# Kernel tuning notes

Measured on AMD Instinct MI355X. Metric: run time of the kernel, lower is better.

## Reference

```python
import jax, jax.numpy as jnp
import numpy as np

N, A, OBS, H, E, ITERS = 2000, 16, 64, 128, 16000, 8


def _init_linear(key, din, dout):
    kw, kb = jax.random.split(key)
    s = 1.0 / np.sqrt(din)
    W = jax.random.uniform(kw, (dout, din), minval=-s, maxval=s, dtype=jnp.float32)
    b = jax.random.uniform(kb, (dout,), minval=-s, maxval=s, dtype=jnp.float32)
    return W, b


def setup_inputs() -> dict:
    key = jax.random.key(0)
    ks = jax.random.split(key, 20)
    x = jax.random.normal(ks[0], (N, OBS), dtype=jnp.float32)
    prev_action = jax.random.normal(ks[1], (N, A), dtype=jnp.float32)
    state = jax.random.normal(ks[2], (1, N, H), dtype=jnp.float32)
    # edges: unique-ish random pairs with i < j (no self loops)
    rng = np.random.default_rng(0)
    ei = rng.integers(0, N - 1, size=E)
    ej = rng.integers(ei + 1, N)
    edges = jnp.asarray(np.stack([ei, ej], axis=1), dtype=jnp.int32)
    # GRU params (torch layout: rows = [r; z; n])
    s = 1.0 / np.sqrt(H)
    gru_wih = jax.random.uniform(ks[3], (3 * H, OBS + A), minval=-s, maxval=s, dtype=jnp.float32)
    gru_whh = jax.random.uniform(ks[4], (3 * H, H), minval=-s, maxval=s, dtype=jnp.float32)
    gru_bih = jax.random.uniform(ks[5], (3 * H,), minval=-s, maxval=s, dtype=jnp.float32)
    gru_bhh = jax.random.uniform(ks[6], (3 * H,), minval=-s, maxval=s, dtype=jnp.float32)
    # utility MLP: [H, 256, 256, A]
    uW0, ub0 = _init_linear(ks[7], H, 256)
    uW1, ub1 = _init_linear(ks[8], 256, 256)
    uW2, ub2 = _init_linear(ks[9], 256, A)
    # payoff MLP: [2H, H, 256, 256, A, A*A]  (faithful to source's dim-list reuse)
    pW0, pb0 = _init_linear(ks[10], 2 * H, H)
    pW1, pb1 = _init_linear(ks[11], H, 256)
    pW2, pb2 = _init_linear(ks[12], 256, 256)
    pW3, pb3 = _init_linear(ks[13], 256, A)
    pW4, pb4 = _init_linear(ks[14], A, A * A)
    return dict(x=x, prev_action=prev_action, state=state, edges=edges,
                gru_wih=gru_wih, gru_whh=gru_whh, gru_bih=gru_bih, gru_bhh=gru_bhh,
                uW0=uW0, ub0=ub0, uW1=uW1, ub1=ub1, uW2=uW2, ub2=ub2,
                pW0=pW0, pb0=pb0, pW1=pW1, pb1=pb1, pW2=pW2, pb2=pb2,
                pW3=pW3, pb3=pb3, pW4=pW4, pb4=pb4)


def _mlp(x, params):
    n = len(params)
    for i, (W, b) in enumerate(params):
        x = x @ W.T + b
        if i < n - 1:
            x = jax.nn.relu(x)
    return x


def _gru_step(inp, h, wih, whh, bih, bhh):
    gi = inp @ wih.T + bih          # [N, 3H]
    gh = h @ whh.T + bhh            # [N, 3H]
    gir, giz, gin = jnp.split(gi, 3, axis=-1)
    ghr, ghz, ghn = jnp.split(gh, 3, axis=-1)
    r = jax.nn.sigmoid(gir + ghr)
    z = jax.nn.sigmoid(giz + ghz)
    n = jnp.tanh(gin + r * ghn)
    return (1.0 - z) * n + z * h


def _message_passing(u, p, ei, ej):
    """u: [N,A] differentiable, p: [E,A,A] differentiable.
    Messages are computed under stop_gradient (torch.no_grad in source);
    Q of the per-iteration greedy action is differentiable in u, p."""
    u_sg = jax.lax.stop_gradient(u)
    p_sg = jax.lax.stop_gradient(p)
    node_idx = jnp.arange(N)
    edge_idx = jnp.arange(E)

    def step(carry, _):
        M, q_max, opt_a = carry            # M[recv, send, A]
        S = M.sum(axis=1)                  # [N, A] total incoming per node
        base_i = u_sg[ei] + S[ei] - M[ei, ej]   # [E, A] indexed by a_i
        base_j = u_sg[ej] + S[ej] - M[ej, ei]   # [E, A] indexed by a_j
        # message i -> j: max over a_i of (p[e,ai,aj] + base_i[ai])
        msg_to_j = (p_sg + base_i[:, :, None]).max(axis=1)   # [E, A]
        msg_to_j = msg_to_j - msg_to_j.mean(axis=-1, keepdims=True)
        # message j -> i (source reduces over dim 0 = a_i; replicated faithfully)
        msg_to_i = (p_sg + base_j[:, None, :]).max(axis=1)   # [E, A]
        msg_to_i = msg_to_i - msg_to_i.mean(axis=-1, keepdims=True)
        M = M.at[ej, ei].set(msg_to_j).at[ei, ej].set(msg_to_i)
        # greedy action per node
        a_idx = jnp.argmax(u_sg + M.sum(axis=1), axis=-1)    # [N]
        q_real = u[node_idx, a_idx].sum() + p[edge_idx, a_idx[ei], a_idx[ej]].sum()
        better = q_real > q_max
        q_max = jnp.where(better, q_real, q_max)
        a_onehot = jax.nn.one_hot(a_idx, A, dtype=u.dtype)
        opt_a = jnp.where(better, a_onehot, opt_a)
        return (M, q_max, opt_a), None

    M0 = jnp.zeros((N, N, A), dtype=u.dtype)
    q0 = jnp.zeros((), dtype=u.dtype)
    a0 = jnp.zeros((N, A), dtype=u.dtype)
    (M, q_max, opt_a), _ = jax.lax.scan(step, (M0, q0, a0), None, length=ITERS)
    return opt_a, q_max


def reference(x, prev_action, state, edges,
              gru_wih, gru_whh, gru_bih, gru_bhh,
              uW0, ub0, uW1, ub1, uW2, ub2,
              pW0, pb0, pW1, pb1, pW2, pb2, pW3, pb3, pW4, pb4):
    ei, ej = edges[:, 0], edges[:, 1]
    enc_in = jnp.concatenate([x, prev_action], axis=-1)        # [N, OBS+A]
    h = _gru_step(enc_in, state[0], gru_wih, gru_whh, gru_bih, gru_bhh)  # [N, H]
    state_out = h.reshape(1, 1, N, H)
    u_params = [(uW0, ub0), (uW1, ub1), (uW2, ub2)]
    p_params = [(pW0, pb0), (pW1, pb1), (pW2, pb2), (pW3, pb3), (pW4, pb4)]
    u = _mlp(h, u_params) / N                                  # [N, A]
    s_ij = jnp.concatenate([h[ei], h[ej]], axis=-1)            # [E, 2H]
    s_ji = jnp.concatenate([h[ej], h[ei]], axis=-1)
    p_ij = _mlp(s_ij, p_params).reshape(E, A, A) / E
    p_ji = _mlp(s_ji, p_params).reshape(E, A, A) / E
    p = 0.5 * (p_ij + p_ji)                                    # [E, A, A]
    a, q_max = _message_passing(u, p, ei, ej)
    return (a, q_max, u[None], p, state_out)
```

## Files before the change

### kernel.cpp

```cpp
#include <hip/hip_runtime.h>
#include <math.h>

#define N_NODES 2000
#define NA 16
#define NOBS 64
#define NH 128
#define NE 16000
#define NITERS 8

#define WS_MSG       0
#define WS_Q         512000
#define WS_SBUF      512016
#define WS_AIDX      800016
#define WS_W         816016
#define WS_PT        832016
#define WS_GIT       (WS_PT + 4000000)
#define WS_GHT       (WS_GIT + 30720)
#define WS_WB        4928016
#define WS_UW0T      (WS_WB + 0)
#define WS_UWCAT     (WS_WB + 32768)
#define WS_UW1T      (WS_WB + 65536)
#define WS_UW2T      (WS_WB + 131072)
#define WS_CAB       (WS_WB + 241664)

#define F16_W1H 0
#define F16_W1L 32768
#define F16_W2H 65536
#define F16_W2L 131072
#define F16_W3H 196608
#define F16_W3L 200704
#define F16_W4H 204800
#define F16_W4L 212992

typedef _Float16 half8 __attribute__((ext_vector_type(8)));
typedef float f32x4 __attribute__((ext_vector_type(4)));

__global__ __launch_bounds__(256) void setup_kernel(
    float* __restrict__ ws, const int* __restrict__ edges,
    const float* __restrict__ uW0, const float* __restrict__ uW1,
    const float* __restrict__ uW2, const float* __restrict__ pW0,
    const float* __restrict__ pW1, const float* __restrict__ pW2,
    const float* __restrict__ pW3, const float* __restrict__ pW4,
    const float* __restrict__ gwih, const float* __restrict__ gwhh)
{
    if (blockIdx.x >= 1024) {
        int e = (blockIdx.x - 1024) * 256 + threadIdx.x;
        if (e < NE) {
            int i = edges[2 * e], j = edges[2 * e + 1];
            ((int*)(ws + WS_PT))[i * N_NODES + j] = -1;
        }
        return;
    }
    const int total = 8 + 135168 + 79872 + 110592;
    for (int idx = blockIdx.x * 256 + threadIdx.x; idx < total;
         idx += 1024 * 256) {
        if (idx < 8) {
            ws[WS_Q + idx] = 0.f;
        } else {
            int t = idx - 8;
            if (t < 135168) {
                float v;
                if (t < 32768) {
                    int k = t / 256, o = t % 256;
                    v = uW0[o * 128 + k];
                } else if (t < 65536) {
                    int q = t - 32768, k = q / 256, o = q % 256;
                    v = (o < 128) ? pW0[o * 256 + k]
                                  : pW0[(o - 128) * 256 + 128 + k];
                } else if (t < 131072) {
                    int q = t - 65536, k = q / 256, o = q % 256;
                    v = uW1[o * 256 + k];
                } else {
                    int q = t - 131072, k = q / 16, o = q % 16;
                    v = uW2[o * 256 + k];
                }
                ws[WS_WB + t] = v;
            } else if (t < 215040) {
                int q = t - 135168;
                if (q < 30720) {
                    int k4 = q / 1536, r = q % 1536, g = r >> 2, c = r & 3;
                    ws[WS_GIT + q] = gwih[g * 80 + 4 * k4 + c];
                } else {
                    int q2 = q - 30720;
                    int k4 = q2 / 1536, r = q2 % 1536, g = r >> 2, c = r & 3;
                    ws[WS_GHT + q2] = gwhh[g * 128 + 4 * k4 + c];
                }
            } else {
                int q = t - 215040;
                _Float16* fw = (_Float16*)ws;
                float v; int hoff, loff;
                if (q < 32768) {
                    v = pW1[q]; hoff = F16_W1H + q; loff = F16_W1L + q;
                } else if (q < 98304) {
                    int z = q - 32768; v = pW2[z];
                    hoff = F16_W2H + z; loff = F16_W2L + z;
                } else if (q < 102400) {
                    int z = q - 98304; v = pW3[z];
                    hoff = F16_W3H + z; loff = F16_W3L + z;
                } else {
                    int z = q - 102400; int n = z >> 5, kk = z & 31;
                    v = (kk < 16) ? pW4[n * 16 + kk] : 0.f;
                    hoff = F16_W4H + z; loff = F16_W4L + z;
                }
                _Float16 hv = (_Float16)v;
                fw[hoff] = hv;
                fw[loff] = (_Float16)(v - (float)hv);
            }
        }
    }
}

__global__ __launch_bounds__(256) void gru_kernel(
    const float* __restrict__ x, const float* __restrict__ pa,
    const float* __restrict__ st, const float* __restrict__ wihT,
    const float* __restrict__ whhT, const float* __restrict__ bih,
    const float* __restrict__ bhh, float* __restrict__ h_out,
    const int* __restrict__ edges, int* __restrict__ owner)
{
    if (blockIdx.x >= 250) {
        int e = (blockIdx.x - 250) * 256 + threadIdx.x;
        if (e < NE) {
            int i = edges[2 * e], j = edges[2 * e + 1];
            atomicMax(&owner[i * N_NODES + j], e);
        }
        return;
    }
    __shared__ float enc[8][80];
    __shared__ float hp[8][128];
    __shared__ float gi[8][384];
    __shared__ float gh[8][384];
    const int tid = threadIdx.x;
    const int n0 = blockIdx.x * 8;

    for (int idx = tid; idx < 8 * 80; idx += 256) {
        int r = idx / 80, c = idx % 80;
        enc[r][c] = (c < 64) ? x[(n0 + r) * 64 + c] : pa[(n0 + r) * 16 + (c - 64)];
    }
    for (int idx = tid; idx < 8 * 128; idx += 256) {
        int r = idx >> 7, c = idx & 127;
        hp[r][c] = st[(n0 + r) * 128 + c];
    }
    __syncthreads();

    for (int idx = tid; idx < 8 * 384; idx += 256) {
        int g = idx % 384, r = idx / 384;
        float s1 = bih[g];
        #pragma unroll 5
        for (int k4 = 0; k4 < 20; ++k4) {
            const float4 ev = *(const float4*)&enc[r][4 * k4];
            const float4 wv = *(const float4*)&wihT[k4 * 1536 + g * 4];
            s1 = fmaf(ev.x, wv.x, fmaf(ev.y, wv.y, fmaf(ev.z, wv.z, fmaf(ev.w, wv.w, s1))));
        }
        gi[r][g] = s1;
        float s2 = bhh[g];
        #pragma unroll 8
        for (int k4 = 0; k4 < 32; ++k4) {
            const float4 hv = *(const float4*)&hp[r][4 * k4];
            const float4 wv = *(const float4*)&whhT[k4 * 1536 + g * 4];
            s2 = fmaf(hv.x, wv.x, fmaf(hv.y, wv.y, fmaf(hv.z, wv.z, fmaf(hv.w, wv.w, s2))));
        }
        gh[r][g] = s2;
    }
    __syncthreads();

    for (int idx = tid; idx < 8 * 128; idx += 256) {
        int r = idx >> 7, c = idx & 127;
        float rr = 1.f / (1.f + expf(-(gi[r][c] + gh[r][c])));
        float zz = 1.f / (1.f + expf(-(gi[r][128 + c] + gh[r][128 + c])));
        float nn = tanhf(gi[r][256 + c] + rr * gh[r][256 + c]);
        h_out[(n0 + r) * 128 + c] = (1.f - zz) * nn + zz * hp[r][c];
    }
}

__global__ __launch_bounds__(256) void umlp_kernel(
    const float* __restrict__ h, const float* __restrict__ w0t,
    const float* __restrict__ b0, const float* __restrict__ w1t,
    const float* __restrict__ b1, const float* __restrict__ w2t,
    const float* __restrict__ b2, const float* __restrict__ wcat,
    float* __restrict__ u_out, float* __restrict__ Sbuf,
    float* __restrict__ cab, const int* __restrict__ edges,
    const int* __restrict__ owner, int* __restrict__ wflag)
{
    if (blockIdx.x >= 500) {
        int e = (blockIdx.x - 500) * 256 + threadIdx.x;
        if (e < NE) {
            int i = edges[2 * e], j = edges[2 * e + 1];
            wflag[e] = (owner[i * N_NODES + j] == e) ? 1 : 0;
        }
        return;
    }
    __shared__ float A[8][128];
    __shared__ float B[8][256];
    const int tid = threadIdx.x;
    const bool is_cab = blockIdx.x >= 250;
    const int n0 = (is_cab ? blockIdx.x - 250 : blockIdx.x) * 8;

    for (int idx = tid; idx < 8 * 128; idx += 256) {
        int r = idx >> 7, c = idx & 127;
        A[r][c] = h[(n0 + r) * 128 + c];
    }
    __syncthreads();

    if (is_cab) {
        const int o = tid;
        const float* wp = wcat + o;
        float wA[4], wB[4];
        #pragma unroll
        for (int c = 0; c < 4; ++c) wA[c] = wp[c * 256];
        float acc[8];
        #pragma unroll
        for (int r = 0; r < 8; ++r) acc[r] = 0.f;
        for (int k4 = 0; k4 < 32; k4 += 2) {
            #pragma unroll
            for (int c = 0; c < 4; ++c) wB[c] = wp[(4 * (k4 + 1) + c) * 256];
            #pragma unroll
            for (int r = 0; r < 8; ++r) {
                const float4 av = *(const float4*)&A[r][4 * k4];
                acc[r] = fmaf(av.x, wA[0], fmaf(av.y, wA[1], fmaf(av.z, wA[2], fmaf(av.w, wA[3], acc[r]))));
            }
            #pragma unroll
            for (int c = 0; c < 4; ++c) wA[c] = wp[(4 * (k4 + 2) + c) * 256];
            #pragma unroll
            for (int r = 0; r < 8; ++r) {
                const float4 av = *(const float4*)&A[r][4 * k4 + 4];
                acc[r] = fmaf(av.x, wB[0], fmaf(av.y, wB[1], fmaf(av.z, wB[2], fmaf(av.w, wB[3], acc[r]))));
            }
        }
        #pragma unroll
        for (int r = 0; r < 8; ++r) cab[(n0 + r) * 256 + o] = acc[r];
        return;
    }

    {
        const int o = tid;
        const float* wp = w0t + o;
        float wA[4], wB[4];
        #pragma unroll
        for (int c = 0; c < 4; ++c) wA[c] = wp[c * 256];
        float acc[8];
        #pragma unroll
        for (int r = 0; r < 8; ++r) acc[r] = b0[o];
        for (int k4 = 0; k4 < 32; k4 += 2) {
            #pragma unroll
            for (int c = 0; c < 4; ++c) wB[c] = wp[(4 * (k4 + 1) + c) * 256];
            #pragma unroll
            for (int r = 0; r < 8; ++r) {
                const float4 av = *(const float4*)&A[r][4 * k4];
                acc[r] = fmaf(av.x, wA[0], fmaf(av.y, wA[1], fmaf(av.z, wA[2], fmaf(av.w, wA[3], acc[r]))));
            }
            #pragma unroll
            for (int c = 0; c < 4; ++c) wA[c] = wp[(4 * (k4 + 2) + c) * 256];
            #pragma unroll
            for (int r = 0; r < 8; ++r) {
                const float4 av = *(const float4*)&A[r][4 * k4 + 4];
                acc[r] = fmaf(av.x, wB[0], fmaf(av.y, wB[1], fmaf(av.z, wB[2], fmaf(av.w, wB[3], acc[r]))));
            }
        }
        #pragma unroll
        for (int r = 0; r < 8; ++r) B[r][o] = fmaxf(acc[r], 0.f);
    }
    __syncthreads();
    {
        const int o = tid;
        const float* wp = w1t + o;
        float wA[4], wB[4];
        #pragma unroll
        for (int c = 0; c < 4; ++c) wA[c] = wp[c * 256];
        float acc[8];
        #pragma unroll
        for (int r = 0; r < 8; ++r) acc[r] = b1[o];
        for (int k4 = 0; k4 < 64; k4 += 2) {
            #pragma unroll
            for (int c = 0; c < 4; ++c) wB[c] = wp[(4 * (k4 + 1) + c) * 256];
            #pragma unroll
            for (int r = 0; r < 8; ++r) {
                const float4 av = *(const float4*)&B[r][4 * k4];
                acc[r] = fmaf(av.x, wA[0], fmaf(av.y, wA[1], fmaf(av.z, wA[2], fmaf(av.w, wA[3], acc[r]))));
            }
            #pragma unroll
            for (int c = 0; c < 4; ++c) wA[c] = wp[(4 * (k4 + 2) + c) * 256];
            #pragma unroll
            for (int r = 0; r < 8; ++r) {
                const float4 av = *(const float4*)&B[r][4 * k4 + 4];
                acc[r] = fmaf(av.x, wB[0], fmaf(av.y, wB[1], fmaf(av.z, wB[2], fmaf(av.w, wB[3], acc[r]))));
            }
        }
        __syncthreads();
        #pragma unroll
        for (int r = 0; r < 8; ++r) B[r][o] = fmaxf(acc[r], 0.f);
    }
    __syncthreads();
    if (tid < 128) {
        int r = tid >> 4, o = tid & 15;
        float acc = b2[o];
        for (int k4 = 0; k4 < 64; ++k4) {
            const float4 av = *(const float4*)&B[r][4 * k4];
            acc = fmaf(av.x, w2t[(4 * k4 + 0) * 16 + o],
                  fmaf(av.y, w2t[(4 * k4 + 1) * 16 + o],
                  fmaf(av.z, w2t[(4 * k4 + 2) * 16 + o],
                  fmaf(av.w, w2t[(4 * k4 + 3) * 16 + o], acc))));
        }
        float val = acc * (1.f / N_NODES);
        int idx = (n0 + r) * 16 + o;
        u_out[idx] = val;
        #pragma unroll
        for (int t = 0; t < NITERS + 1; ++t) Sbuf[t * 32000 + idx] = val;
    }
}

__global__ __launch_bounds__(256, 4) void pmlp_kernel(
    const float* __restrict__ cab, const int* __restrict__ edges,
    const float* __restrict__ b0, const _Float16* __restrict__ fw,
    const float* __restrict__ b1, const float* __restrict__ b2,
    const float* __restrict__ b3, const float* __restrict__ b4,
    float* __restrict__ p_out, float* __restrict__ pT)
{
    __shared__ __align__(16) _Float16 Ah[32][264];
    __shared__ __align__(16) _Float16 Al[32][264];
    __shared__ float C16[32][16];
    __shared__ float redC[2][32][16];
    __shared__ int fi[32], se[32];

    const int tid  = threadIdx.x;
    const int e0   = blockIdx.x * 16;
    const int wid  = tid >> 6;
    const int lane = tid & 63;
    const int lrow = lane & 15;
    const int lgrp = lane >> 4;
    const int koff = 8 * lgrp;

    if (tid < 16) {
        int i = edges[2 * (e0 + tid)], j = edges[2 * (e0 + tid) + 1];
        fi[2 * tid] = i;     se[2 * tid] = j;
        fi[2 * tid + 1] = j; se[2 * tid + 1] = i;
    }
    __syncthreads();

    {
        const int cl = tid & 127;
        const int rh = tid >> 7;
        const float bb = b0[cl];
        #pragma unroll 4
        for (int r = rh * 16; r < rh * 16 + 16; ++r) {
            float v = cab[fi[r] * 256 + cl] + cab[se[r] * 256 + 128 + cl] + bb;
            v = fmaxf(v, 0.f);
            _Float16 hv = (_Float16)v;
            Ah[r][cl] = hv;
            Al[r][cl] = (_Float16)(v - (float)hv);
        }
    }
    __syncthreads();

    f32x4 acc[2][4];

    #pragma unroll
    for (int mt = 0; mt < 2; ++mt)
        #pragma unroll
        for (int nt = 0; nt < 4; ++nt) acc[mt][nt] = (f32x4){0.f, 0.f, 0.f, 0.f};
    #pragma unroll
    for (int ks = 0; ks < 4; ++ks) {
        half8 ah[2], al[2];
        #pragma unroll
        for (int mt = 0; mt < 2; ++mt) {
            ah[mt] = *(const half8*)&Ah[16 * mt + lrow][32 * ks + koff];
            al[mt] = *(const half8*)&Al[16 * mt + lrow][32 * ks + koff];
        }
        #pragma unroll
        for (int nt = 0; nt < 4; ++nt) {
            const int n = 64 * wid + 16 * nt + lrow;
            half8 bh = *(const half8*)(fw + F16_W1H + n * 128 + 32 * ks + koff);
            half8 bl = *(const half8*)(fw + F16_W1L + n * 128 + 32 * ks + koff);
            #pragma unroll
            for (int mt = 0; mt < 2; ++mt) {
                acc[mt][nt] = __builtin_amdgcn_mfma_f32_16x16x32_f16(ah[mt], bh, acc[mt][nt], 0, 0, 0);
                acc[mt][nt] = __builtin_amdgcn_mfma_f32_16x16x32_f16(ah[mt], bl, acc[mt][nt], 0, 0, 0);
                acc[mt][nt] = __builtin_amdgcn_mfma_f32_16x16x32_f16(al[mt], bh, acc[mt][nt], 0, 0, 0);
            }
        }
    }
    __syncthreads();
    #pragma unroll
    for (int nt = 0; nt < 4; ++nt) {
        const int col = 64 * wid + 16 * nt + lrow;
        const float bv = b1[col];
        #pragma unroll
        for (int mt = 0; mt < 2; ++mt) {
            #pragma unroll
            for (int r = 0; r < 4; ++r) {
                const int row = 16 * mt + 4 * lgrp + r;
                float v = fmaxf(acc[mt][nt][r] + bv, 0.f);
                _Float16 hv = (_Float16)v;
                Ah[row][col] = hv;
                Al[row][col] = (_Float16)(v - (float)hv);
            }
        }
    }
    __syncthreads();

    #pragma unroll
    for (int mt = 0; mt < 2; ++mt)
        #pragma unroll
        for (int nt = 0; nt < 4; ++nt) acc[mt][nt] = (f32x4){0.f, 0.f, 0.f, 0.f};
    for (int ks = 0; ks < 8; ++ks) {
        half8 ah[2], al[2];
        #pragma unroll
        for (int mt = 0; mt < 2; ++mt) {
            ah[mt] = *(const half8*)&Ah[16 * mt + lrow][32 * ks + koff];
            al[mt] = *(const half8*)&Al[16 * mt + lrow][32 * ks + koff];
        }
        #pragma unroll
        for (int nt = 0; nt < 4; ++nt) {
            const int n = 64 * wid + 16 * nt + lrow;
            half8 bh = *(const half8*)(fw + F16_W2H + n * 256 + 32 * ks + koff);
            half8 bl = *(const half8*)(fw + F16_W2L + n * 256 + 32 * ks + koff);
            #pragma unroll
            for (int mt = 0; mt < 2; ++mt) {
                acc[mt][nt] = __builtin_amdgcn_mfma_f32_16x16x32_f16(ah[mt], bh, acc[mt][nt], 0, 0, 0);
                acc[mt][nt] = __builtin_amdgcn_mfma_f32_16x16x32_f16(ah[mt], bl, acc[mt][nt], 0, 0, 0);
                acc[mt][nt] = __builtin_amdgcn_mfma_f32_16x16x32_f16(al[mt], bh, acc[mt][nt], 0, 0, 0);
            }
        }
    }
    __syncthreads();
    #pragma unroll
    for (int nt = 0; nt < 4; ++nt) {
        const int col = 64 * wid + 16 * nt + lrow;
        const float bv = b2[col];
        #pragma unroll
        for (int mt = 0; mt < 2; ++mt) {
            #pragma unroll
            for (int r = 0; r < 4; ++r) {
                const int row = 16 * mt + 4 * lgrp + r;
                float v = fmaxf(acc[mt][nt][r] + bv, 0.f);
                _Float16 hv = (_Float16)v;
                Ah[row][col] = hv;
                Al[row][col] = (_Float16)(v - (float)hv);
            }
        }
    }
    __syncthreads();

    {
        const int mt = wid & 1, kh = wid >> 1;
        f32x4 acc3 = {0.f, 0.f, 0.f, 0.f};
        #pragma unroll
        for (int ks = 4 * kh; ks < 4 * kh + 4; ++ks) {
            half8 ah = *(const half8*)&Ah[16 * mt + lrow][32 * ks + koff];
            half8 al = *(const half8*)&Al[16 * mt + lrow][32 * ks + koff];
            half8 bh = *(const half8*)(fw + F16_W3H + lrow * 256 + 32 * ks + koff);
            half8 bl = *(const half8*)(fw + F16_W3L + lrow * 256 + 32 * ks + koff);
            acc3 = __builtin_amdgcn_mfma_f32_16x16x32_f16(ah, bh, acc3, 0, 0, 0);
            acc3 = __builtin_amdgcn_mfma_f32_16x16x32_f16(ah, bl, acc3, 0, 0, 0);
            acc3 = __builtin_amdgcn_mfma_f32_16x16x32_f16(al, bh, acc3, 0, 0, 0);
        }
        #pragma unroll
        for (int r = 0; r < 4; ++r)
            redC[kh][16 * mt + 4 * lgrp + r][lrow] = acc3[r];
    }
    __syncthreads();
    for (int idx = tid; idx < 512; idx += 256) {
        int r = idx >> 4, o = idx & 15;
        C16[r][o] = fmaxf(redC[0][r][o] + redC[1][r][o] + b3[o], 0.f);
    }
    __syncthreads();

    {
        half8 a4h[2], a4l[2];
        #pragma unroll
        for (int mt = 0; mt < 2; ++mt) {
            half8 hh, ll;
            #pragma unroll
            for (int j = 0; j < 8; ++j) { hh[j] = (_Float16)0.f; ll[j] = (_Float16)0.f; }
            if (lgrp < 2) {
                #pragma unroll
                for (int j = 0; j < 8; ++j) {
                    float v = C16[16 * mt + lrow][8 * lgrp + j];
                    _Float16 hv = (_Float16)v;
                    hh[j] = hv;
                    ll[j] = (_Float16)(v - (float)hv);
                }
            }
            a4h[mt] = hh; a4l[mt] = ll;
        }
        #pragma unroll
        for (int nt = 0; nt < 4; ++nt) {
            const int o = 64 * wid + 16 * nt + lrow;
            const float b4v = b4[o];
            half8 bh = *(const half8*)(fw + F16_W4H + o * 32 + koff);
            half8 bl = *(const half8*)(fw + F16_W4L + o * 32 + koff);
            const int ot = (o & 15) * 16 + (o >> 4);
            #pragma unroll
            for (int mt = 0; mt < 2; ++mt) {
                f32x4 a4 = {0.f, 0.f, 0.f, 0.f};
                a4 = __builtin_amdgcn_mfma_f32_16x16x32_f16(a4h[mt], bh, a4, 0, 0, 0);
                a4 = __builtin_amdgcn_mfma_f32_16x16x32_f16(a4h[mt], bl, a4, 0, 0, 0);
                a4 = __builtin_amdgcn_mfma_f32_16x16x32_f16(a4l[mt], bh, a4, 0, 0, 0);
                const int s0 = 8 * mt + 2 * lgrp;
                float pa = (0.5f * (a4[0] + a4[1]) + b4v) * (1.f / NE);
                float pb = (0.5f * (a4[2] + a4[3]) + b4v) * (1.f / NE);
                p_out[(e0 + s0) * 256 + o] = pa;
                p_out[(e0 + s0 + 1) * 256 + o] = pb;
                pT[(e0 + s0) * 256 + ot] = pa;
                pT[(e0 + s0 + 1) * 256 + ot] = pb;
            }
        }
    }
}

__global__ __launch_bounds__(256) void mp_iter_kernel(
    const float* __restrict__ u, float* __restrict__ Sbuf,
    float* __restrict__ msg, const float* __restrict__ pT,
    const float* __restrict__ p, const int* __restrict__ edges,
    const int* __restrict__ wflag, int* __restrict__ aidx,
    float* __restrict__ q, int t)
{
    const int tid = threadIdx.x;
    if (blockIdx.x < 500) {
        const int g = blockIdx.x * 16 + (tid >> 4);
        const int L = tid & 15;
        const int eA = g, eB = g + 8000;
        const float* uSo = Sbuf + t * 32000;
        float* uSn = Sbuf + (t + 1) * 32000;
        const int iA = edges[2 * eA], jA = edges[2 * eA + 1];
        const int iB = edges[2 * eB], jB = edges[2 * eB + 1];
        float moldA_ij = 0.f, moldA_ji = 0.f, moldB_ij = 0.f, moldB_ji = 0.f;
        if (t > 0) {
            moldA_ij = msg[(NE + eA) * 16 + L];
            moldA_ji = msg[eA * 16 + L];
            moldB_ij = msg[(NE + eB) * 16 + L];
            moldB_ji = msg[eB * 16 + L];
        }
        const float biA = uSo[iA * 16 + L] - moldA_ij;
        const float bjA = uSo[jA * 16 + L] - moldA_ji;
        const float biB = uSo[iB * 16 + L] - moldB_ij;
        const float bjB = uSo[jB * 16 + L] - moldB_ji;
        const float4* ptA = (const float4*)(pT + eA * 256 + L * 16);
        const float4* ptB = (const float4*)(pT + eB * 256 + L * 16);
        const float4 a0 = ptA[0], a1 = ptA[1], a2 = ptA[2], a3 = ptA[3];
        const float4 c0 = ptB[0], c1 = ptB[1], c2 = ptB[2], c3 = ptB[3];
        float pvA[16] = {a0.x, a0.y, a0.z, a0.w, a1.x, a1.y, a1.z, a1.w,
                         a2.x, a2.y, a2.z, a2.w, a3.x, a3.y, a3.z, a3.w};
        float pvB[16] = {c0.x, c0.y, c0.z, c0.w, c1.x, c1.y, c1.z, c1.w,
                         c2.x, c2.y, c2.z, c2.w, c3.x, c3.y, c3.z, c3.w};
        float mjA = -INFINITY, vmaxA = -INFINITY;
        float mjB = -INFINITY, vmaxB = -INFINITY;
        #pragma unroll
        for (int a = 0; a < 16; ++a) {
            float biaA = __shfl(biA, a, 16);
            float biaB = __shfl(biB, a, 16);
            mjA = fmaxf(mjA, pvA[a] + biaA);
            vmaxA = fmaxf(vmaxA, pvA[a]);
            mjB = fmaxf(mjB, pvB[a] + biaB);
            vmaxB = fmaxf(vmaxB, pvB[a]);
        }
        float miA = vmaxA + bjA;
        float miB = vmaxB + bjB;
        float sjA = mjA, siA = miA, sjB = mjB, siB = miB;
        #pragma unroll
        for (int off = 1; off < 16; off <<= 1) {
            sjA += __shfl_xor(sjA, off, 16);
            siA += __shfl_xor(siA, off, 16);
            sjB += __shfl_xor(sjB, off, 16);
            siB += __shfl_xor(siB, off, 16);
        }
        mjA -= sjA * (1.f / 16.f);
        miA -= siA * (1.f / 16.f);
        mjB -= sjB * (1.f / 16.f);
        miB -= siB * (1.f / 16.f);
        msg[eA * 16 + L] = mjA;
        msg[(NE + eA) * 16 + L] = miA;
        msg[eB * 16 + L] = mjB;
        msg[(NE + eB) * 16 + L] = miB;
        if (wflag[eA]) {
            atomicAdd(&uSn[jA * 16 + L], mjA);
            atomicAdd(&uSn[iA * 16 + L], miA);
        }
        if (wflag[eB]) {
            atomicAdd(&uSn[jB * 16 + L], mjB);
            atomicAdd(&uSn[iB * 16 + L], miB);
        }
    } else if (t > 0) {
        const int r = (blockIdx.x - 500) * 256 + tid;
        const float* Sn = Sbuf + t * 32000;
        float partial = 0.f;
        if (r < N_NODES) {
            int n = r;
            float bv = Sn[n * 16];
            int best = 0;
            #pragma unroll
            for (int a = 1; a < 16; ++a) {
                float v = Sn[n * 16 + a];
                if (v > bv) { bv = v; best = a; }
            }
            aidx[(t - 1) * N_NODES + n] = best;
            partial = u[n * 16 + best];
        } else if (r < N_NODES + NE) {
            int ee = r - N_NODES;
            int ii = edges[2 * ee], jj = edges[2 * ee + 1];
            float bvi = Sn[ii * 16]; int ai = 0;
            #pragma unroll
            for (int a = 1; a < 16; ++a) {
                float v = Sn[ii * 16 + a];
                if (v > bvi) { bvi = v; ai = a; }
            }
            float bvj = Sn[jj * 16]; int aj = 0;
            #pragma unroll
            for (int a = 1; a < 16; ++a) {
                float v = Sn[jj * 16 + a];
                if (v > bvj) { bvj = v; aj = a; }
            }
            partial = p[ee * 256 + ai * 16 + aj];
        }
        #pragma unroll
        for (int off = 1; off < 64; off <<= 1) partial += __shfl_xor(partial, off, 64);
        if ((tid & 63) == 0) atomicAdd(&q[t - 1], partial);
    }
}

__global__ __launch_bounds__(256) void mp_tail_kernel(
    const float* __restrict__ u, const float* __restrict__ Sbuf,
    const float* __restrict__ p, const int* __restrict__ edges,
    int* __restrict__ aidx, float* __restrict__ q)
{
    const int tid = threadIdx.x;
    const int r = blockIdx.x * 256 + tid;
    const float* Sn = Sbuf + NITERS * 32000;
    float partial = 0.f;
    if (r < N_NODES) {
        int n = r;
        float bv = Sn[n * 16];
        int best = 0;
        #pragma unroll
        for (int a = 1; a < 16; ++a) {
            float v = Sn[n * 16 + a];
            if (v > bv) { bv = v; best = a; }
        }
        aidx[(NITERS - 1) * N_NODES + n] = best;
        partial = u[n * 16 + best];
    } else if (r < N_NODES + NE) {
        int ee = r - N_NODES;
        int ii = edges[2 * ee], jj = edges[2 * ee + 1];
        float bvi = Sn[ii * 16]; int ai = 0;
        #pragma unroll
        for (int a = 1; a < 16; ++a) {
            float v = Sn[ii * 16 + a];
            if (v > bvi) { bvi = v; ai = a; }
        }
        float bvj = Sn[jj * 16]; int aj = 0;
        #pragma unroll
        for (int a = 1; a < 16; ++a) {
            float v = Sn[jj * 16 + a];
            if (v > bvj) { bvj = v; aj = a; }
        }
        partial = p[ee * 256 + ai * 16 + aj];
    }
    #pragma unroll
    for (int off = 1; off < 64; off <<= 1) partial += __shfl_xor(partial, off, 64);
    if ((tid & 63) == 0) atomicAdd(&q[NITERS - 1], partial);
}

__global__ __launch_bounds__(256) void final_kernel(
    const float* __restrict__ q, const int* __restrict__ aidx,
    float* __restrict__ a_out, float* __restrict__ q_out)
{
    int id = blockIdx.x * 256 + threadIdx.x;
    float cur = 0.f; int best_t = -1;
    #pragma unroll
    for (int t = 0; t < NITERS; ++t) {
        float qv = q[t];
        if (qv > cur) { cur = qv; best_t = t; }
    }
    if (id < N_NODES * 16) {
        int n = id >> 4, c = id & 15;
        float val = 0.f;
        if (best_t >= 0 && aidx[best_t * N_NODES + n] == c) val = 1.f;
        a_out[id] = val;
        if (id == 0) q_out[0] = cur;
    }
}

extern "C" void kernel_launch(void* const* d_in, const int* in_sizes, int n_in,
                              void* d_out, int out_size, void* d_ws, size_t ws_size,
                              hipStream_t stream)
{
    (void)in_sizes; (void)n_in; (void)out_size; (void)ws_size;
    const float* x    = (const float*)d_in[0];
    const float* pa   = (const float*)d_in[1];
    const float* st   = (const float*)d_in[2];
    const int*   edges= (const int*)d_in[3];
    const float* gwih = (const float*)d_in[4];
    const float* gwhh = (const float*)d_in[5];
    const float* gbih = (const float*)d_in[6];
    const float* gbhh = (const float*)d_in[7];
    const float* uW0 = (const float*)d_in[8];  const float* ub0 = (const float*)d_in[9];
    const float* uW1 = (const float*)d_in[10]; const float* ub1 = (const float*)d_in[11];
    const float* uW2 = (const float*)d_in[12]; const float* ub2 = (const float*)d_in[13];
    const float* pW0 = (const float*)d_in[14]; const float* pb0 = (const float*)d_in[15];
    const float* pW1 = (const float*)d_in[16]; const float* pb1 = (const float*)d_in[17];
    const float* pW2 = (const float*)d_in[18]; const float* pb2 = (const float*)d_in[19];
    const float* pW3 = (const float*)d_in[20]; const float* pb3 = (const float*)d_in[21];
    const float* pW4 = (const float*)d_in[22]; const float* pb4 = (const float*)d_in[23];

    float* out   = (float*)d_out;
    float* a_out = out;
    float* q_out = out + 32000;
    float* u_out = out + 32001;
    float* p_out = out + 64001;
    float* h_out = out + 4160001;

    float* ws   = (float*)d_ws;
    float* msg  = ws + WS_MSG;
    float* Sbuf = ws + WS_SBUF;
    float* q    = ws + WS_Q;
    int*   aidx = (int*)(ws + WS_AIDX);
    int*   wfl  = (int*)(ws + WS_W);
    float* pT   = ws + WS_PT;
    float* cab  = ws + WS_CAB;
    int*   owner= (int*)(ws + WS_PT);

    setup_kernel<<<1087, 256, 0, stream>>>(ws, edges, uW0, uW1, uW2,
                                           pW0, pW1, pW2, pW3, pW4, gwih, gwhh);
    gru_kernel<<<313, 256, 0, stream>>>(x, pa, st, ws + WS_GIT, ws + WS_GHT,
                                        gbih, gbhh, h_out, edges, owner);
    umlp_kernel<<<563, 256, 0, stream>>>(h_out, ws + WS_UW0T, ub0,
                                         ws + WS_UW1T, ub1, ws + WS_UW2T, ub2,
                                         ws + WS_UWCAT, u_out, Sbuf, cab,
                                         edges, owner, wfl);
    pmlp_kernel<<<NE / 16, 256, 0, stream>>>(cab, edges, pb0,
                                             (const _Float16*)ws,
                                             pb1, pb2, pb3, pb4, p_out, pT);
    for (int t = 0; t < NITERS; ++t) {
        mp_iter_kernel<<<571, 256, 0, stream>>>(u_out, Sbuf, msg, pT, p_out,
                                                edges, wfl, aidx, q, t);
    }
    mp_tail_kernel<<<71, 256, 0, stream>>>(u_out, Sbuf, p_out, edges, aidx, q);
    final_kernel<<<125, 256, 0, stream>>>(q, aidx, a_out, q_out);
}
```

Measured before the change: 305.7 us.

## Fuse message-passing iterations into one persistent kernel with grid barriers

```diff
diff --git a/kernel.cpp b/kernel.cpp
--- a/kernel.cpp
+++ b/kernel.cpp
@@ -51,13 +51,13 @@
         }
         return;
     }
-    const int total = 8 + 135168 + 79872 + 110592;
+    const int total = 16 + 135168 + 79872 + 110592;
     for (int idx = blockIdx.x * 256 + threadIdx.x; idx < total;
          idx += 1024 * 256) {
-        if (idx < 8) {
+        if (idx < 16) {
             ws[WS_Q + idx] = 0.f;
         } else {
-            int t = idx - 8;
+            int t = idx - 16;
             if (t < 135168) {
                 float v;
                 if (t < 32768) {
@@ -75,7 +75,7 @@
                     v = uW2[o * 256 + k];
                 }
                 ws[WS_WB + t] = v;
-            } else if (t < 215040) {
+            } else if (t < 215056) {
                 int q = t - 135168;
                 if (q < 30720) {
                     int k4 = q / 1536, r = q % 1536, g = r >> 2, c = r & 3;
@@ -86,7 +86,8 @@
                     ws[WS_GHT + q2] = gwhh[g * 128 + 4 * k4 + c];
                 }
             } else {
-                int q = t - 215040;
+                int q = t - 215056;
+                if (q >= 110592) continue;
                 _Float16* fw = (_Float16*)ws;
                 float v; int hoff, loff;
                 if (q < 32768) {
@@ -507,175 +508,129 @@
     }
 }
 
-__global__ __launch_bounds__(256) void mp_iter_kernel(
+__device__ __forceinline__ void grid_bar(int* cnt, int* gen, int nb)
+{
+    __syncthreads();
+    if (threadIdx.x == 0) {
+        __threadfence();
+        int g = __hip_atomic_load(gen, __ATOMIC_RELAXED, __HIP_MEMORY_SCOPE_AGENT);
+        int old = __hip_atomic_fetch_add(cnt, 1, __ATOMIC_ACQ_REL, __HIP_MEMORY_SCOPE_AGENT);
+        if (old == nb - 1) {
+            __hip_atomic_store(cnt, 0, __ATOMIC_RELAXED, __HIP_MEMORY_SCOPE_AGENT);
+            __hip_atomic_fetch_add(gen, 1, __ATOMIC_RELEASE, __HIP_MEMORY_SCOPE_AGENT);
+        } else {
+            while (__hip_atomic_load(gen, __ATOMIC_RELAXED, __HIP_MEMORY_SCOPE_AGENT) == g)
+                __builtin_amdgcn_s_sleep(2);
+        }
+        __threadfence();
+    }
+    __syncthreads();
+}
+
+__global__ __launch_bounds__(512, 4) void mp_fused_kernel(
     const float* __restrict__ u, float* __restrict__ Sbuf,
-    float* __restrict__ msg, const float* __restrict__ pT,
-    const float* __restrict__ p, const int* __restrict__ edges,
-    const int* __restrict__ wflag, int* __restrict__ aidx,
-    float* __restrict__ q, int t)
+    const float* __restrict__ pT, const float* __restrict__ p,
+    const int* __restrict__ edges, const int* __restrict__ wflag,
+    int* __restrict__ aidx, float* __restrict__ q,
+    float* __restrict__ a_out, float* __restrict__ q_out,
+    int* __restrict__ bar)
 {
     const int tid = threadIdx.x;
-    if (blockIdx.x < 500) {
-        const int g = blockIdx.x * 16 + (tid >> 4);
-        const int L = tid & 15;
-        const int eA = g, eB = g + 8000;
-        const float* uSo = Sbuf + t * 32000;
-        float* uSn = Sbuf + (t + 1) * 32000;
-        const int iA = edges[2 * eA], jA = edges[2 * eA + 1];
-        const int iB = edges[2 * eB], jB = edges[2 * eB + 1];
-        float moldA_ij = 0.f, moldA_ji = 0.f, moldB_ij = 0.f, moldB_ji = 0.f;
-        if (t > 0) {
-            moldA_ij = msg[(NE + eA) * 16 + L];
-            moldA_ji = msg[eA * 16 + L];
-            moldB_ij = msg[(NE + eB) * 16 + L];
-            moldB_ji = msg[eB * 16 + L];
-        }
-        const float biA = uSo[iA * 16 + L] - moldA_ij;
-        const float bjA = uSo[jA * 16 + L] - moldA_ji;
-        const float biB = uSo[iB * 16 + L] - moldB_ij;
-        const float bjB = uSo[jB * 16 + L] - moldB_ji;
-        const float4* ptA = (const float4*)(pT + eA * 256 + L * 16);
-        const float4* ptB = (const float4*)(pT + eB * 256 + L * 16);
-        const float4 a0 = ptA[0], a1 = ptA[1], a2 = ptA[2], a3 = ptA[3];
-        const float4 c0 = ptB[0], c1 = ptB[1], c2 = ptB[2], c3 = ptB[3];
-        float pvA[16] = {a0.x, a0.y, a0.z, a0.w, a1.x, a1.y, a1.z, a1.w,
-                         a2.x, a2.y, a2.z, a2.w, a3.x, a3.y, a3.z, a3.w};
-        float pvB[16] = {c0.x, c0.y, c0.z, c0.w, c1.x, c1.y, c1.z, c1.w,
-                         c2.x, c2.y, c2.z, c2.w, c3.x, c3.y, c3.z, c3.w};
-        float mjA = -INFINITY, vmaxA = -INFINITY;
-        float mjB = -INFINITY, vmaxB = -INFINITY;
-        #pragma unroll
-        for (int a = 0; a < 16; ++a) {
-            float biaA = __shfl(biA, a, 16);
-            float biaB = __shfl(biB, a, 16);
-            mjA = fmaxf(mjA, pvA[a] + biaA);
-            vmaxA = fmaxf(vmaxA, pvA[a]);
-            mjB = fmaxf(mjB, pvB[a] + biaB);
-            vmaxB = fmaxf(vmaxB, pvB[a]);
-        }
-        float miA = vmaxA + bjA;
-        float miB = vmaxB + bjB;
-        float sjA = mjA, siA = miA, sjB = mjB, siB = miB;
-        #pragma unroll
-        for (int off = 1; off < 16; off <<= 1) {
-            sjA += __shfl_xor(sjA, off, 16);
-            siA += __shfl_xor(siA, off, 16);
-            sjB += __shfl_xor(sjB, off, 16);
-            siB += __shfl_xor(siB, off, 16);
-        }
-        mjA -= sjA * (1.f / 16.f);
-        miA -= siA * (1.f / 16.f);
-        mjB -= sjB * (1.f / 16.f);
-        miB -= siB * (1.f / 16.f);
-        msg[eA * 16 + L] = mjA;
-        msg[(NE + eA) * 16 + L] = miA;
-        msg[eB * 16 + L] = mjB;
-        msg[(NE + eB) * 16 + L] = miB;
-        if (wflag[eA]) {
-            atomicAdd(&uSn[jA * 16 + L], mjA);
-            atomicAdd(&uSn[iA * 16 + L], miA);
-        }
-        if (wflag[eB]) {
-            atomicAdd(&uSn[jB * 16 + L], mjB);
-            atomicAdd(&uSn[iB * 16 + L], miB);
-        }
-    } else if (t > 0) {
-        const int r = (blockIdx.x - 500) * 256 + tid;
-        const float* Sn = Sbuf + t * 32000;
-        float partial = 0.f;
-        if (r < N_NODES) {
-            int n = r;
-            float bv = Sn[n * 16];
-            int best = 0;
-            #pragma unroll
-            for (int a = 1; a < 16; ++a) {
-                float v = Sn[n * 16 + a];
-                if (v > bv) { bv = v; best = a; }
-            }
-            aidx[(t - 1) * N_NODES + n] = best;
-            partial = u[n * 16 + best];
-        } else if (r < N_NODES + NE) {
-            int ee = r - N_NODES;
-            int ii = edges[2 * ee], jj = edges[2 * ee + 1];
-            float bvi = Sn[ii * 16]; int ai = 0;
-            #pragma unroll
-            for (int a = 1; a < 16; ++a) {
-                float v = Sn[ii * 16 + a];
-                if (v > bvi) { bvi = v; ai = a; }
-            }
-            float bvj = Sn[jj * 16]; int aj = 0;
-            #pragma unroll
-            for (int a = 1; a < 16; ++a) {
-                float v = Sn[jj * 16 + a];
-                if (v > bvj) { bvj = v; aj = a; }
-            }
-            partial = p[ee * 256 + ai * 16 + aj];
-        }
-        #pragma unroll
-        for (int off = 1; off < 64; off <<= 1) partial += __shfl_xor(partial, off, 64);
-        if ((tid & 63) == 0) atomicAdd(&q[t - 1], partial);
-    }
-}
-
-__global__ __launch_bounds__(256) void mp_tail_kernel(
-    const float* __restrict__ u, const float* __restrict__ Sbuf,
-    const float* __restrict__ p, const int* __restrict__ edges,
-    int* __restrict__ aidx, float* __restrict__ q)
-{
-    const int tid = threadIdx.x;
-    const int r = blockIdx.x * 256 + tid;
-    const float* Sn = Sbuf + NITERS * 32000;
-    float partial = 0.f;
-    if (r < N_NODES) {
-        int n = r;
-        float bv = Sn[n * 16];
-        int best = 0;
-        #pragma unroll
-        for (int a = 1; a < 16; ++a) {
-            float v = Sn[n * 16 + a];
-            if (v > bv) { bv = v; best = a; }
-        }
-        aidx[(NITERS - 1) * N_NODES + n] = best;
-        partial = u[n * 16 + best];
-    } else if (r < N_NODES + NE) {
-        int ee = r - N_NODES;
-        int ii = edges[2 * ee], jj = edges[2 * ee + 1];
-        float bvi = Sn[ii * 16]; int ai = 0;
-        #pragma unroll
-        for (int a = 1; a < 16; ++a) {
-            float v = Sn[ii * 16 + a];
-            if (v > bvi) { bvi = v; ai = a; }
-        }
-        float bvj = Sn[jj * 16]; int aj = 0;
-        #pragma unroll
-        for (int a = 1; a < 16; ++a) {
-            float v = Sn[jj * 16 + a];
-            if (v > bvj) { bvj = v; aj = a; }
-        }
-        partial = p[ee * 256 + ai * 16 + aj];
-    }
+    const int bid = blockIdx.x;
+    const int e   = bid * 32 + (tid >> 4);
+    const int L   = tid & 15;
+    const int r   = bid * 512 + tid;
+    int* cnt = bar;
+    int* gen = bar + 1;
+
+    const int gi = edges[2 * e], gj = edges[2 * e + 1];
+    const int wf = wflag[e];
+    const float4* pt = (const float4*)(pT + e * 256 + L * 16);
+    const float4 p0 = pt[0], p1 = pt[1], p2 = pt[2], p3 = pt[3];
+    float pv[16] = {p0.x, p0.y, p0.z, p0.w, p1.x, p1.y, p1.z, p1.w,
+                    p2.x, p2.y, p2.z, p2.w, p3.x, p3.y, p3.z, p3.w};
+    float vmax = -INFINITY;
     #pragma unroll
-    for (int off = 1; off < 64; off <<= 1) partial += __shfl_xor(partial, off, 64);
-    if ((tid & 63) == 0) atomicAdd(&q[NITERS - 1], partial);
-}
-
-__global__ __launch_bounds__(256) void final_kernel(
-    const float* __restrict__ q, const int* __restrict__ aidx,
-    float* __restrict__ a_out, float* __restrict__ q_out)
-{
-    int id = blockIdx.x * 256 + threadIdx.x;
-    float cur = 0.f; int best_t = -1;
-    #pragma unroll
-    for (int t = 0; t < NITERS; ++t) {
-        float qv = q[t];
-        if (qv > cur) { cur = qv; best_t = t; }
-    }
-    if (id < N_NODES * 16) {
-        int n = id >> 4, c = id & 15;
+    for (int a = 0; a < 16; ++a) vmax = fmaxf(vmax, pv[a]);
+    float mold_ij = 0.f, mold_ji = 0.f;
+
+    for (int t = 0; t <= NITERS; ++t) {
+        if (t) grid_bar(cnt, gen, 500);
+        if (t < NITERS) {
+            const float* uSo = Sbuf + t * 32000;
+            float* uSn = Sbuf + (t + 1) * 32000;
+            const float bi = uSo[gi * 16 + L] - mold_ij;
+            const float bj = uSo[gj * 16 + L] - mold_ji;
+            float mj = -INFINITY;
+            #pragma unroll
+            for (int a = 0; a < 16; ++a)
+                mj = fmaxf(mj, pv[a] + __shfl(bi, a, 16));
+            float mi = vmax + bj;
+            float sj = mj, si = mi;
+            #pragma unroll
+            for (int off = 1; off < 16; off <<= 1) {
+                sj += __shfl_xor(sj, off, 16);
+                si += __shfl_xor(si, off, 16);
+            }
+            mj -= sj * (1.f / 16.f);
+            mi -= si * (1.f / 16.f);
+            mold_ji = mj;
+            mold_ij = mi;
+            if (wf) {
+                atomicAdd(&uSn[gj * 16 + L], mj);
+                atomicAdd(&uSn[gi * 16 + L], mi);
+            }
+        }
+        if (t > 0 && bid < 36) {
+            const float* Sn = Sbuf + t * 32000;
+            float partial = 0.f;
+            if (r < N_NODES) {
+                int n = r;
+                float bv = Sn[n * 16];
+                int best = 0;
+                #pragma unroll
+                for (int a = 1; a < 16; ++a) {
+                    float v = Sn[n * 16 + a];
+                    if (v > bv) { bv = v; best = a; }
+                }
+                aidx[(t - 1) * N_NODES + n] = best;
+                partial = u[n * 16 + best];
+            } else if (r < N_NODES + NE) {
+                int ee = r - N_NODES;
+                int ii = edges[2 * ee], jj = edges[2 * ee + 1];
+                float bvi = Sn[ii * 16]; int ai = 0;
+                #pragma unroll
+                for (int a = 1; a < 16; ++a) {
+                    float v = Sn[ii * 16 + a];
+                    if (v > bvi) { bvi = v; ai = a; }
+                }
+                float bvj = Sn[jj * 16]; int aj = 0;
+                #pragma unroll
+                for (int a = 1; a < 16; ++a) {
+                    float v = Sn[jj * 16 + a];
+                    if (v > bvj) { bvj = v; aj = a; }
+                }
+                partial = p[ee * 256 + ai * 16 + aj];
+            }
+            #pragma unroll
+            for (int off = 1; off < 64; off <<= 1)
+                partial += __shfl_xor(partial, off, 64);
+            if ((tid & 63) == 0) atomicAdd(&q[t - 1], partial);
+        }
+    }
+    grid_bar(cnt, gen, 500);
+    if (r < N_NODES * 16) {
+        float cur = 0.f; int best_t = -1;
+        #pragma unroll
+        for (int t2 = 0; t2 < NITERS; ++t2) {
+            float qv = q[t2];
+            if (qv > cur) { cur = qv; best_t = t2; }
+        }
+        int n = r >> 4, c = r & 15;
         float val = 0.f;
         if (best_t >= 0 && aidx[best_t * N_NODES + n] == c) val = 1.f;
-        a_out[id] = val;
-        if (id == 0) q_out[0] = cur;
+        a_out[r] = val;
+        if (r == 0) q_out[0] = cur;
     }
 }
 
@@ -709,9 +664,9 @@
     float* h_out = out + 4160001;
 
     float* ws   = (float*)d_ws;
-    float* msg  = ws + WS_MSG;
     float* Sbuf = ws + WS_SBUF;
     float* q    = ws + WS_Q;
+    int*   bar  = (int*)(ws + WS_Q + 8);
     int*   aidx = (int*)(ws + WS_AIDX);
     int*   wfl  = (int*)(ws + WS_W);
     float* pT   = ws + WS_PT;
@@ -729,10 +684,7 @@
     pmlp_kernel<<<NE / 16, 256, 0, stream>>>(cab, edges, pb0,
                                              (const _Float16*)ws,
                                              pb1, pb2, pb3, pb4, p_out, pT);
-    for (int t = 0; t < NITERS; ++t) {
-        mp_iter_kernel<<<571, 256, 0, stream>>>(u_out, Sbuf, msg, pT, p_out,
-                                                edges, wfl, aidx, q, t);
-    }
-    mp_tail_kernel<<<71, 256, 0, stream>>>(u_out, Sbuf, p_out, edges, aidx, q);
-    final_kernel<<<125, 256, 0, stream>>>(q, aidx, a_out, q_out);
+    mp_fused_kernel<<<500, 512, 0, stream>>>(u_out, Sbuf, pT, p_out,
+                                             edges, wfl, aidx, q,
+                                             a_out, q_out, bar);
 }
```

Measured after the change: 852.2 us. +178.8%, slower.
